# Optimization experiments

Measured on AMD Instinct MI355X. Metric: run time of the kernel, lower is better.

Reference implementation:

```python
import jax, jax.numpy as jnp
import numpy as np

# Mamba hyperparameters (match init_kwargs)
DIM = 384
D_STATE = 16
D_CONV = 4
EXPAND = 2
D_INNER = EXPAND * DIM            # 768
DT_RANK = (DIM + 15) // 16        # ceil(dim/16) = 24


def setup_inputs() -> dict:
    key = jax.random.key(0)
    ks = jax.random.split(key, 9)
    B = 4
    img_dims = (16, 16, 16)
    s = 0.02
    x = jax.random.normal(ks[0], (B, DIM) + img_dims, dtype=jnp.float32)
    # LayerNorm params
    gamma = jnp.ones((DIM,), jnp.float32)
    beta = jnp.zeros((DIM,), jnp.float32)
    # Mamba params (torch Linear layout: (out, in))
    W_in = jax.random.normal(ks[1], (2 * D_INNER, DIM), jnp.float32) * s
    conv_w = jax.random.normal(ks[2], (D_INNER, 1, D_CONV), jnp.float32) * (D_CONV ** -0.5)
    conv_b = jnp.zeros((D_INNER,), jnp.float32)
    W_xproj = jax.random.normal(ks[3], (DT_RANK + 2 * D_STATE, D_INNER), jnp.float32) * s
    W_dt = jax.random.normal(ks[4], (D_INNER, DT_RANK), jnp.float32) * (DT_RANK ** -0.5)
    # bias init so softplus(b_dt) gives small positive dt (~0.02), like mamba_ssm
    b_dt = jnp.full((D_INNER,), -4.0, jnp.float32) + jax.random.normal(ks[5], (D_INNER,), jnp.float32) * 0.1
    # S4D-real init: A = -[1..d_state] per channel
    A_log = jnp.log(jnp.broadcast_to(jnp.arange(1, D_STATE + 1, dtype=jnp.float32), (D_INNER, D_STATE)))
    D = jnp.ones((D_INNER,), jnp.float32)
    W_out = jax.random.normal(ks[6], (DIM, D_INNER), jnp.float32) * s
    return {"x": x, "gamma": gamma, "beta": beta, "W_in": W_in, "conv_w": conv_w,
            "conv_b": conv_b, "W_xproj": W_xproj, "W_dt": W_dt, "b_dt": b_dt,
            "A_log": A_log, "D": D, "W_out": W_out}


def _mamba_layer(x, gamma, beta, W_in, conv_w, conv_b, W_xproj, W_dt, b_dt, A_log, D, W_out):
    B, C = x.shape[0], x.shape[1]
    img_dims = x.shape[2:]
    L = int(np.prod(img_dims))
    xf = x.reshape(B, C, L).transpose(0, 2, 1)          # (B, L, C)

    # LayerNorm over channel dim
    mu = xf.mean(-1, keepdims=True)
    xc = xf - mu
    var = (xc * xc).mean(-1, keepdims=True)
    xn = xc * jax.lax.rsqrt(var + 1e-5) * gamma + beta   # (B, L, C)

    # in_proj -> x, z branches
    xz = xn @ W_in.T                                     # (B, L, 2*D_INNER)
    xm, z = jnp.split(xz, 2, axis=-1)

    # causal depthwise conv1d + SiLU
    xcv = xm.transpose(0, 2, 1)                          # (B, D_INNER, L)
    conv = jax.lax.conv_general_dilated(
        xcv, conv_w, window_strides=(1,), padding=[(D_CONV - 1, 0)],
        feature_group_count=D_INNER) + conv_b[None, :, None]
    xm = jax.nn.silu(conv.transpose(0, 2, 1))            # (B, L, D_INNER)

    # input-dependent dt, B, C
    dbl = xm @ W_xproj.T                                 # (B, L, DT_RANK + 2*D_STATE)
    dt, Bm, Cm = jnp.split(dbl, [DT_RANK, DT_RANK + D_STATE], axis=-1)
    delta = jax.nn.softplus(dt @ W_dt.T + b_dt)          # (B, L, D_INNER)
    A = -jnp.exp(A_log)                                  # (D_INNER, D_STATE)

    # selective scan over time (time-major)
    def step(h, inp):
        d_t, x_t, B_t, C_t = inp                         # (B,Din),(B,Din),(B,Dst),(B,Dst)
        dA = jnp.exp(d_t[..., None] * A)                 # (B, D_INNER, D_STATE)
        h = h * dA + (d_t * x_t)[..., None] * B_t[:, None, :]
        y = jnp.einsum('bds,bs->bd', h, C_t)
        return h, y

    h0 = jnp.zeros((B, D_INNER, D_STATE), xm.dtype)
    inps = (delta.transpose(1, 0, 2), xm.transpose(1, 0, 2),
            Bm.transpose(1, 0, 2), Cm.transpose(1, 0, 2))
    _, ys = jax.lax.scan(step, h0, inps)                 # (L, B, D_INNER)

    y = ys.transpose(1, 0, 2) + xm * D                   # skip via D
    y = y * jax.nn.silu(z)                               # gate
    out = y @ W_out.T                                    # (B, L, C)
    return out.transpose(0, 2, 1).reshape(x.shape)


def reference(x, gamma, beta, W_in, conv_w, conv_b, W_xproj, W_dt, b_dt, A_log, D, W_out):
    return _mamba_layer(x, gamma, beta, W_in, conv_w, conv_b, W_xproj, W_dt, b_dt, A_log, D, W_out)
```

## Files before the change

kernel.cpp:

```cpp
#include <hip/hip_runtime.h>

typedef short v8s __attribute__((ext_vector_type(8)));
typedef float v4f __attribute__((ext_vector_type(4)));

#define LSEQ   4096
#define BATCH  4
#define NDIM   384
#define DIN    768
#define DST    16
#define DTR    24
#define NTOK   (BATCH * LSEQ)
#define NCHUNK 128
#define CLEN   32
#define CT     8

__device__ __forceinline__ float b2f(unsigned short u) {
  unsigned int v = ((unsigned int)u) << 16;
  float f; __builtin_memcpy(&f, &v, 4); return f;
}
__device__ __forceinline__ unsigned short f2b(float f) {
  unsigned int x; __builtin_memcpy(&x, &f, 4);
  unsigned int r = x + 0x7FFFu + ((x >> 16) & 1u);
  return (unsigned short)(r >> 16);
}
__device__ __forceinline__ void gl2lds16(const void* g, void* l) {
  __builtin_amdgcn_global_load_lds(
      (const __attribute__((address_space(1))) void*)g,
      (__attribute__((address_space(3))) void*)l, 16, 0, 0);
}

__global__ __launch_bounds__(256) void cast_w(
    const float* __restrict__ a, unsigned short* __restrict__ oa, int na,
    const float* __restrict__ b, unsigned short* __restrict__ ob, int nb,
    const float* __restrict__ c, unsigned short* __restrict__ oc, int nc,
    const float* __restrict__ wdt, unsigned short* __restrict__ odt)
{
  int i = blockIdx.x * 256 + threadIdx.x;
  if (i < na) oa[i] = f2b(a[i]);
  if (i < nb) ob[i] = f2b(b[i]);
  if (i < nc) oc[i] = f2b(c[i]);
  if (i < DIN * 32) {
    int n = i >> 5, r = i & 31;
    odt[i] = (r < DTR) ? f2b(wdt[n * DTR + r]) : (unsigned short)0;
  }
}

__global__ __launch_bounds__(256) void ln_stats(
    const float* __restrict__ x, float* __restrict__ mu, float* __restrict__ rs)
{
  __shared__ float red[512];
  int blk = blockIdx.x;
  int b = blk >> 7, lc = blk & 127;
  int l0 = lc * 32;
  int t = threadIdx.x;
  int lt = t & 31, part = t >> 5;
  float s = 0.f, ss = 0.f;
  for (int c = part; c < NDIM; c += 8) {
    float v = x[((size_t)b * NDIM + c) * LSEQ + l0 + lt];
    s += v; ss += v * v;
  }
  red[part * 32 + lt] = s;
  red[256 + part * 32 + lt] = ss;
  __syncthreads();
  if (t < 32) {
    float sum = 0.f, ssum = 0.f;
    #pragma unroll
    for (int k = 0; k < 8; k++) { sum += red[k * 32 + t]; ssum += red[256 + k * 32 + t]; }
    float m = sum / (float)NDIM;
    float var = ssum / (float)NDIM - m * m;
    mu[(size_t)b * LSEQ + l0 + t] = m;
    rs[(size_t)b * LSEQ + l0 + t] = rsqrtf(var + 1e-5f);
  }
}

__global__ __launch_bounds__(256) void ln_apply(
    const float* __restrict__ x, const float* __restrict__ mu,
    const float* __restrict__ rs, const float* __restrict__ gamma,
    const float* __restrict__ beta, unsigned short* __restrict__ xn)
{
  __shared__ unsigned short tile[64 * 66];
  int blk = blockIdx.x;
  int ltb = blk & 63, ct = (blk >> 6) % 6, b = blk / (6 * 64);
  int l0 = ltb * 64, c0 = ct * 64;
  int t = threadIdx.x;
  int col = (t & 15) * 4;
  float4 mu4 = *(const float4*)(mu + (size_t)b * LSEQ + l0 + col);
  float4 rs4 = *(const float4*)(rs + (size_t)b * LSEQ + l0 + col);
  #pragma unroll
  for (int p = 0; p < 4; p++) {
    int row = (t >> 4) + p * 16;
    float g = gamma[c0 + row], be = beta[c0 + row];
    float4 v = *(const float4*)(x + ((size_t)b * NDIM + c0 + row) * LSEQ + l0 + col);
    unsigned int u0 = (unsigned int)f2b((v.x - mu4.x) * rs4.x * g + be)
                    | ((unsigned int)f2b((v.y - mu4.y) * rs4.y * g + be) << 16);
    unsigned int u1 = (unsigned int)f2b((v.z - mu4.z) * rs4.z * g + be)
                    | ((unsigned int)f2b((v.w - mu4.w) * rs4.w * g + be) << 16);
    *(unsigned int*)&tile[row * 66 + col]     = u0;
    *(unsigned int*)&tile[row * 66 + col + 2] = u1;
  }
  __syncthreads();
  for (int idx = t; idx < 64 * 64; idx += 256) {
    int l = idx >> 6, c = idx & 63;
    xn[((size_t)b * LSEQ + l0 + l) * NDIM + c0 + c] = tile[c * 66 + l];
  }
}

template <typename OT>
__global__ __launch_bounds__(256) void gemm128(
    const unsigned short* __restrict__ A, const unsigned short* __restrict__ W,
    OT* __restrict__ C, int K, int ldc)
{
  __shared__ short As[128 * 32];
  __shared__ short Ws[128 * 32];
  int t = threadIdx.x;
  int wave = t >> 6, lane = t & 63;
  int m0 = blockIdx.x * 128, n0 = blockIdx.y * 128;
  int wm = wave >> 1, wn = wave & 1;
  int lrow = lane & 15, quad = lane >> 4;
  int l4 = lane >> 2, p = lane & 3;
  int row0 = wave * 32 + l4;
  int row1 = row0 + 16;
  int k8 = p ^ (row0 & 3);
  int ldsoff0 = wave * 1024 + lane * 8;
  int ldsoff1 = ldsoff0 + 512;
  int swz = (lrow & 3) * 8;
  v4f acc[4][4];
  #pragma unroll
  for (int i = 0; i < 4; i++)
    #pragma unroll
    for (int j = 0; j < 4; j++) acc[i][j] = (v4f){0.f, 0.f, 0.f, 0.f};
  for (int kk = 0; kk < K; kk += 32) {
    gl2lds16(A + (size_t)(m0 + row0) * K + kk + k8 * 8, &As[ldsoff0]);
    gl2lds16(A + (size_t)(m0 + row1) * K + kk + k8 * 8, &As[ldsoff1]);
    gl2lds16(W + (size_t)(n0 + row0) * K + kk + k8 * 8, &Ws[ldsoff0]);
    gl2lds16(W + (size_t)(n0 + row1) * K + kk + k8 * 8, &Ws[ldsoff1]);
    __syncthreads();
    v8s af[4], bf[4];
    #pragma unroll
    for (int i = 0; i < 4; i++) {
      int ra = wm * 64 + i * 16 + lrow;
      af[i] = *(const v8s*)&As[ra * 32 + ((quad * 8) ^ swz)];
    }
    #pragma unroll
    for (int j = 0; j < 4; j++) {
      int rb = wn * 64 + j * 16 + lrow;
      bf[j] = *(const v8s*)&Ws[rb * 32 + ((quad * 8) ^ swz)];
    }
    #pragma unroll
    for (int i = 0; i < 4; i++)
      #pragma unroll
      for (int j = 0; j < 4; j++)
        acc[i][j] = __builtin_amdgcn_mfma_f32_16x16x32_bf16(af[i], bf[j], acc[i][j], 0, 0, 0);
    __syncthreads();
  }
  #pragma unroll
  for (int i = 0; i < 4; i++) {
    #pragma unroll
    for (int j = 0; j < 4; j++) {
      #pragma unroll
      for (int r = 0; r < 4; r++) {
        int m = m0 + wm * 64 + i * 16 + quad * 4 + r;
        int n = n0 + wn * 64 + j * 16 + lrow;
        if constexpr (sizeof(OT) == 4) C[(size_t)m * ldc + n] = acc[i][j][r];
        else                           C[(size_t)m * ldc + n] = (OT)f2b(acc[i][j][r]);
      }
    }
  }
}

#define LDK 40
__global__ __launch_bounds__(256) void gemm_bt64(
    const unsigned short* __restrict__ A, const unsigned short* __restrict__ W,
    unsigned short* __restrict__ C, int Nw, int K, int ldc)
{
  __shared__ short As[64 * LDK];
  __shared__ short Ws[64 * LDK];
  int m0 = blockIdx.x * 64, n0 = blockIdx.y * 64;
  int t = threadIdx.x;
  int wave = t >> 6, lane = t & 63;
  int lrow = lane & 15, quad = lane >> 4;
  int ldrow = t >> 2, ldcg = t & 3;
  v4f acc[4];
  #pragma unroll
  for (int j = 0; j < 4; j++) acc[j] = (v4f){0.f, 0.f, 0.f, 0.f};
  for (int kk = 0; kk < K; kk += 32) {
    v8s av = *(const v8s*)(A + (size_t)(m0 + ldrow) * K + kk + ldcg * 8);
    *(v8s*)&As[ldrow * LDK + ldcg * 8] = av;
    int wrow = n0 + ldrow;
    v8s wv = {0, 0, 0, 0, 0, 0, 0, 0};
    if (wrow < Nw) wv = *(const v8s*)(W + (size_t)wrow * K + kk + ldcg * 8);
    *(v8s*)&Ws[ldrow * LDK + ldcg * 8] = wv;
    __syncthreads();
    v8s afrag = *(const v8s*)&As[(wave * 16 + lrow) * LDK + quad * 8];
    #pragma unroll
    for (int j = 0; j < 4; j++) {
      v8s bfrag = *(const v8s*)&Ws[(j * 16 + lrow) * LDK + quad * 8];
      acc[j] = __builtin_amdgcn_mfma_f32_16x16x32_bf16(afrag, bfrag, acc[j], 0, 0, 0);
    }
    __syncthreads();
  }
  #pragma unroll
  for (int j = 0; j < 4; j++) {
    #pragma unroll
    for (int r = 0; r < 4; r++) {
      int m = m0 + wave * 16 + quad * 4 + r;
      int n = n0 + j * 16 + lrow;
      if (n < ldc) C[(size_t)m * ldc + n] = f2b(acc[j][r]);
    }
  }
}

__global__ __launch_bounds__(256) void dt_gemm(
    const unsigned short* __restrict__ A, const unsigned short* __restrict__ W,
    const float* __restrict__ b_dt, unsigned short* __restrict__ delta)
{
  __shared__ short As[128 * 32];
  __shared__ short Ws[128 * 32];
  int t = threadIdx.x;
  int wave = t >> 6, lane = t & 63;
  int m0 = blockIdx.x * 128, n0 = blockIdx.y * 128;
  int wm = wave >> 1, wn = wave & 1;
  int lrow = lane & 15, quad = lane >> 4;
  int l4 = lane >> 2, p = lane & 3;
  int row0 = wave * 32 + l4;
  int row1 = row0 + 16;
  int k8 = p ^ (row0 & 3);
  int ldsoff0 = wave * 1024 + lane * 8;
  int ldsoff1 = ldsoff0 + 512;
  int swz = (lrow & 3) * 8;
  gl2lds16(A + (size_t)(m0 + row0) * 64 + k8 * 8, &As[ldsoff0]);
  gl2lds16(A + (size_t)(m0 + row1) * 64 + k8 * 8, &As[ldsoff1]);
  gl2lds16(W + (size_t)(n0 + row0) * 32 + k8 * 8, &Ws[ldsoff0]);
  gl2lds16(W + (size_t)(n0 + row1) * 32 + k8 * 8, &Ws[ldsoff1]);
  __syncthreads();
  v4f acc[4][4];
  #pragma unroll
  for (int i = 0; i < 4; i++)
    #pragma unroll
    for (int j = 0; j < 4; j++) acc[i][j] = (v4f){0.f, 0.f, 0.f, 0.f};
  v8s af[4], bf[4];
  #pragma unroll
  for (int i = 0; i < 4; i++) {
    int ra = wm * 64 + i * 16 + lrow;
    af[i] = *(const v8s*)&As[ra * 32 + ((quad * 8) ^ swz)];
  }
  #pragma unroll
  for (int j = 0; j < 4; j++) {
    int rb = wn * 64 + j * 16 + lrow;
    bf[j] = *(const v8s*)&Ws[rb * 32 + ((quad * 8) ^ swz)];
  }
  #pragma unroll
  for (int i = 0; i < 4; i++)
    #pragma unroll
    for (int j = 0; j < 4; j++)
      acc[i][j] = __builtin_amdgcn_mfma_f32_16x16x32_bf16(af[i], bf[j], acc[i][j], 0, 0, 0);
  #pragma unroll
  for (int j = 0; j < 4; j++) {
    int n = n0 + wn * 64 + j * 16 + lrow;
    float bb = b_dt[n];
    #pragma unroll
    for (int i = 0; i < 4; i++) {
      #pragma unroll
      for (int r = 0; r < 4; r++) {
        int m = m0 + wm * 64 + i * 16 + quad * 4 + r;
        float a = acc[i][j][r] + bb;
        float sp = (a > 20.f) ? a : __logf(1.f + __expf(a));
        delta[(size_t)m * DIN + n] = f2b(sp);
      }
    }
  }
}

__global__ __launch_bounds__(256) void conv_silu_w(
    const unsigned short* __restrict__ xz, const float* __restrict__ conv_w,
    const float* __restrict__ conv_b, unsigned short* __restrict__ xc)
{
  int idx = blockIdx.x * 256 + threadIdx.x;
  int dg = idx % (DIN / 8);
  int bl0 = idx / (DIN / 8);
  int d = dg * 8;
  int t0 = bl0 * CT;
  int l0 = t0 & (LSEQ - 1);
  float w[4][8], bb[8];
  #pragma unroll
  for (int e = 0; e < 8; e++) {
    float4 we = *(const float4*)(conv_w + (size_t)(d + e) * 4);
    w[0][e] = we.x; w[1][e] = we.y; w[2][e] = we.z; w[3][e] = we.w;
  }
  {
    float4 b0 = *(const float4*)(conv_b + d);
    float4 b1 = *(const float4*)(conv_b + d + 4);
    bb[0] = b0.x; bb[1] = b0.y; bb[2] = b0.z; bb[3] = b0.w;
    bb[4] = b1.x; bb[5] = b1.y; bb[6] = b1.z; bb[7] = b1.w;
  }
  float xw[3][8];
  #pragma unroll
  for (int j = 0; j < 3; j++) {
    if (l0 - 3 + j >= 0) {
      v8s v = *(const v8s*)(xz + (size_t)(t0 - 3 + j) * (2 * DIN) + d);
      #pragma unroll
      for (int e = 0; e < 8; e++) xw[j][e] = b2f((unsigned short)v[e]);
    } else {
      #pragma unroll
      for (int e = 0; e < 8; e++) xw[j][e] = 0.f;
    }
  }
  for (int tt = 0; tt < CT; tt++) {
    v8s v = *(const v8s*)(xz + (size_t)(t0 + tt) * (2 * DIN) + d);
    float cur[8];
    #pragma unroll
    for (int e = 0; e < 8; e++) cur[e] = b2f((unsigned short)v[e]);
    v8s o;
    #pragma unroll
    for (int e = 0; e < 8; e++) {
      float acc = bb[e];
      acc = __builtin_fmaf(w[0][e], xw[0][e], acc);
      acc = __builtin_fmaf(w[1][e], xw[1][e], acc);
      acc = __builtin_fmaf(w[2][e], xw[2][e], acc);
      acc = __builtin_fmaf(w[3][e], cur[e], acc);
      float sig = 1.f / (1.f + __expf(-acc));
      o[e] = (short)f2b(acc * sig);
    }
    *(v8s*)(xc + (size_t)(t0 + tt) * DIN + d) = o;
    #pragma unroll
    for (int e = 0; e < 8; e++) {
      xw[0][e] = xw[1][e]; xw[1][e] = xw[2][e]; xw[2][e] = cur[e];
    }
  }
}

__global__ __launch_bounds__(256) void scan_a(
    const unsigned short* __restrict__ delta, const unsigned short* __restrict__ xc,
    const unsigned short* __restrict__ dbl, const float* __restrict__ A_log,
    float* __restrict__ P, float* __restrict__ H)
{
  __shared__ float BCf[CLEN * 32];
  int blk = blockIdx.x;
  int q = blk % 3, c = (blk / 3) % NCHUNK, b = blk / (3 * NCHUNK);
  int t = threadIdx.x;
  int d = q * 256 + t;
  if (t < CLEN * 4) {
    int tt = t >> 2, g = t & 3;
    v8s raw = *(const v8s*)(dbl + (size_t)(b * LSEQ + c * CLEN + tt) * 64 + DTR + g * 8);
    float* dst = &BCf[tt * 32 + g * 8];
    #pragma unroll
    for (int e = 0; e < 8; e++) dst[e] = b2f((unsigned short)raw[e]);
  }
  __syncthreads();
  float A_d[DST];
  bool fast = true;
  #pragma unroll
  for (int s = 0; s < DST; s++) {
    A_d[s] = -__expf(A_log[d * DST + s]);
    fast = fast && (__builtin_fabsf(A_d[s] + (float)(s + 1)) < 1e-3f * (s + 1));
  }
  float h[DST];
  #pragma unroll
  for (int s = 0; s < DST; s++) h[s] = 0.f;
  float S = 0.f;
  size_t base = ((size_t)b * LSEQ + c * CLEN) * DIN + d;
  if (fast) {
    for (int tt = 0; tt < CLEN; tt++) {
      float du = b2f(delta[base + (size_t)tt * DIN]);
      float xv = b2f(xc[base + (size_t)tt * DIN]);
      float dx = du * xv;
      S += du;
      float r = __expf(-du);
      float Bv[16];
      #pragma unroll
      for (int g = 0; g < 4; g++)
        *(float4*)&Bv[g * 4] = *(const float4*)&BCf[tt * 32 + g * 4];
      float a = r;
      #pragma unroll
      for (int s = 0; s < DST; s++) {
        h[s] = __builtin_fmaf(h[s], a, dx * Bv[s]);
        a *= r;
      }
    }
  } else {
    for (int tt = 0; tt < CLEN; tt++) {
      float du = b2f(delta[base + (size_t)tt * DIN]);
      float xv = b2f(xc[base + (size_t)tt * DIN]);
      float dx = du * xv;
      S += du;
      #pragma unroll
      for (int s = 0; s < DST; s++) {
        float a = __expf(du * A_d[s]);
        h[s] = h[s] * a + dx * BCf[tt * 32 + s];
      }
    }
  }
  size_t obase = (((size_t)b * NCHUNK + c) * DST) * DIN + d;
  if (fast) {
    float rS = __expf(-S), a = rS;
    #pragma unroll
    for (int s = 0; s < DST; s++) { P[obase + (size_t)s * DIN] = a; a *= rS; }
  } else {
    #pragma unroll
    for (int s = 0; s < DST; s++) P[obase + (size_t)s * DIN] = __expf(A_d[s] * S);
  }
  #pragma unroll
  for (int s = 0; s < DST; s++) H[obase + (size_t)s * DIN] = h[s];
}

__global__ __launch_bounds__(256) void scan_b(
    const float* __restrict__ P, const float* __restrict__ H, float* __restrict__ Hstart)
{
  int i = blockIdx.x * 256 + threadIdx.x;
  if (i >= BATCH * DST * DIN) return;
  int d = i % DIN;
  int s = (i / DIN) % DST;
  int b = i / (DST * DIN);
  float h = 0.f;
  for (int c = 0; c < NCHUNK; c++) {
    size_t idx = (((size_t)b * NCHUNK + c) * DST + s) * DIN + d;
    float p = P[idx];
    float hh = H[idx];
    Hstart[idx] = h;
    h = h * p + hh;
  }
}

__global__ __launch_bounds__(256) void scan_c(
    const unsigned short* __restrict__ delta, const unsigned short* __restrict__ xc,
    const unsigned short* __restrict__ dbl, const float* __restrict__ A_log,
    const float* __restrict__ Hstart, const unsigned short* __restrict__ xz,
    const float* __restrict__ Dp, unsigned short* __restrict__ ygate)
{
  __shared__ float BCf[CLEN * 32];
  int blk = blockIdx.x;
  int q = blk % 3, c = (blk / 3) % NCHUNK, b = blk / (3 * NCHUNK);
  int t = threadIdx.x;
  int d = q * 256 + t;
  if (t < CLEN * 4) {
    int tt = t >> 2, g = t & 3;
    v8s raw = *(const v8s*)(dbl + (size_t)(b * LSEQ + c * CLEN + tt) * 64 + DTR + g * 8);
    float* dst = &BCf[tt * 32 + g * 8];
    #pragma unroll
    for (int e = 0; e < 8; e++) dst[e] = b2f((unsigned short)raw[e]);
  }
  __syncthreads();
  float A_d[DST];
  bool fast = true;
  #pragma unroll
  for (int s = 0; s < DST; s++) {
    A_d[s] = -__expf(A_log[d * DST + s]);
    fast = fast && (__builtin_fabsf(A_d[s] + (float)(s + 1)) < 1e-3f * (s + 1));
  }
  size_t obase = (((size_t)b * NCHUNK + c) * DST) * DIN + d;
  float h[DST];
  #pragma unroll
  for (int s = 0; s < DST; s++) h[s] = Hstart[obase + (size_t)s * DIN];
  float Dv = Dp[d];
  size_t base = ((size_t)b * LSEQ + c * CLEN) * DIN + d;
  size_t zbase = ((size_t)b * LSEQ + c * CLEN) * (2 * DIN) + DIN + d;
  if (fast) {
    for (int tt = 0; tt < CLEN; tt++) {
      float du = b2f(delta[base + (size_t)tt * DIN]);
      float xv = b2f(xc[base + (size_t)tt * DIN]);
      float dx = du * xv;
      float r = __expf(-du);
      float Bv[16], Cv[16];
      #pragma unroll
      for (int g = 0; g < 4; g++) {
        *(float4*)&Bv[g * 4] = *(const float4*)&BCf[tt * 32 + g * 4];
        *(float4*)&Cv[g * 4] = *(const float4*)&BCf[tt * 32 + 16 + g * 4];
      }
      float a = r, y = 0.f;
      #pragma unroll
      for (int s = 0; s < DST; s++) {
        h[s] = __builtin_fmaf(h[s], a, dx * Bv[s]);
        y = __builtin_fmaf(h[s], Cv[s], y);
        a *= r;
      }
      float zv = b2f(xz[zbase + (size_t)tt * (2 * DIN)]);
      float g = zv / (1.f + __expf(-zv));
      float o = (y + xv * Dv) * g;
      ygate[base + (size_t)tt * DIN] = f2b(o);
    }
  } else {
    for (int tt = 0; tt < CLEN; tt++) {
      float du = b2f(delta[base + (size_t)tt * DIN]);
      float xv = b2f(xc[base + (size_t)tt * DIN]);
      float dx = du * xv;
      float y = 0.f;
      #pragma unroll
      for (int s = 0; s < DST; s++) {
        float a = __expf(du * A_d[s]);
        h[s] = h[s] * a + dx * BCf[tt * 32 + s];
        y += h[s] * BCf[tt * 32 + 16 + s];
      }
      float zv = b2f(xz[zbase + (size_t)tt * (2 * DIN)]);
      float g = zv / (1.f + __expf(-zv));
      float o = (y + xv * Dv) * g;
      ygate[base + (size_t)tt * DIN] = f2b(o);
    }
  }
}

__global__ __launch_bounds__(256) void transpose_out(
    const float* __restrict__ ytmp, float* __restrict__ out)
{
  __shared__ float tl[64][65];
  int blk = blockIdx.x;
  int ct = blk % 6, lt = (blk / 6) % 64, b = blk / (6 * 64);
  int t = threadIdx.x;
  int col = t & 63, row = t >> 6;
  for (int i = row; i < 64; i += 4)
    tl[i][col] = ytmp[((size_t)b * LSEQ + lt * 64 + i) * NDIM + ct * 64 + col];
  __syncthreads();
  for (int i = row; i < 64; i += 4)
    out[((size_t)b * NDIM + ct * 64 + i) * LSEQ + lt * 64 + col] = tl[col][i];
}

extern "C" void kernel_launch(void* const* d_in, const int* in_sizes, int n_in,
                              void* d_out, int out_size, void* d_ws, size_t ws_size,
                              hipStream_t stream) {
  const float* x      = (const float*)d_in[0];
  const float* gamma  = (const float*)d_in[1];
  const float* beta   = (const float*)d_in[2];
  const float* W_in   = (const float*)d_in[3];
  const float* conv_w = (const float*)d_in[4];
  const float* conv_b = (const float*)d_in[5];
  const float* W_xprj = (const float*)d_in[6];
  const float* W_dt   = (const float*)d_in[7];
  const float* b_dt   = (const float*)d_in[8];
  const float* A_log  = (const float*)d_in[9];
  const float* Dp     = (const float*)d_in[10];
  const float* W_out  = (const float*)d_in[11];
  float* out = (float*)d_out;

  char* ws = (char*)d_ws;
  size_t off = 0;
  auto take = [&](size_t bytes) -> char* {
    char* p = ws + off;
    off = (off + bytes + 255) & ~(size_t)255;
    return p;
  };
  const int NW_IN = 2 * DIN * NDIM;
  const int NW_XP = 56 * DIN;
  const int NW_OUT = NDIM * DIN;
  unsigned short* Wc_in  = (unsigned short*)take((size_t)NW_IN * 2);
  unsigned short* Wc_xp  = (unsigned short*)take((size_t)NW_XP * 2);
  unsigned short* Wc_out = (unsigned short*)take((size_t)NW_OUT * 2);
  unsigned short* Wc_dt  = (unsigned short*)take((size_t)DIN * 32 * 2);
  float*          mu    = (float*)take((size_t)NTOK * 4);
  float*          rsb   = (float*)take((size_t)NTOK * 4);
  unsigned short* xn    = (unsigned short*)take((size_t)NTOK * NDIM * 2);
  unsigned short* xz    = (unsigned short*)take((size_t)NTOK * 2 * DIN * 2);
  unsigned short* xc    = (unsigned short*)take((size_t)NTOK * DIN * 2);
  unsigned short* dbl   = (unsigned short*)take((size_t)NTOK * 64 * 2);
  unsigned short* delta = (unsigned short*)take((size_t)NTOK * DIN * 2);
  unsigned short* ygate = (unsigned short*)take((size_t)NTOK * DIN * 2);
  float*          P     = (float*)take((size_t)BATCH * NCHUNK * DST * DIN * 4);
  float*          H     = (float*)take((size_t)BATCH * NCHUNK * DST * DIN * 4);
  float*          Hst   = P;
  float*          ytmp  = (float*)delta;
  (void)ws_size; (void)in_sizes; (void)n_in; (void)out_size;

  cast_w<<<(NW_IN + 255) / 256, 256, 0, stream>>>(W_in, Wc_in, NW_IN,
                                                  W_xprj, Wc_xp, NW_XP,
                                                  W_out, Wc_out, NW_OUT,
                                                  W_dt, Wc_dt);
  ln_stats<<<BATCH * (LSEQ / 32), 256, 0, stream>>>(x, mu, rsb);
  ln_apply<<<BATCH * 6 * (LSEQ / 64), 256, 0, stream>>>(x, mu, rsb, gamma, beta, xn);
  gemm128<unsigned short><<<dim3(NTOK / 128, 1536 / 128), 256, 0, stream>>>(xn, Wc_in, xz, NDIM, 1536);
  conv_silu_w<<<(NTOK / CT) * (DIN / 8) / 256, 256, 0, stream>>>(xz, conv_w, conv_b, xc);
  gemm_bt64<<<dim3(NTOK / 64, 1), 256, 0, stream>>>(xc, Wc_xp, dbl, 56, DIN, 64);
  dt_gemm<<<dim3(NTOK / 128, DIN / 128), 256, 0, stream>>>(dbl, Wc_dt, b_dt, delta);
  scan_a<<<BATCH * NCHUNK * 3, 256, 0, stream>>>(delta, xc, dbl, A_log, P, H);
  scan_b<<<(BATCH * DST * DIN + 255) / 256, 256, 0, stream>>>(P, H, Hst);
  scan_c<<<BATCH * NCHUNK * 3, 256, 0, stream>>>(delta, xc, dbl, A_log, Hst, xz, Dp, ygate);
  gemm128<float><<<dim3(NTOK / 128, NDIM / 128), 256, 0, stream>>>(ygate, Wc_out, ytmp, DIN, NDIM);
  transpose_out<<<BATCH * 64 * 6, 256, 0, stream>>>(ytmp, out);
}
```

Measured before the change: 315.0 us.

## Fuse output transpose into out-proj GEMM and process two channels per scan thread

Adds a gemm_out kernel that computes W_out·ygateᵀ with swapped operands and writes straight into the channel-major output layout, which removes the fp32 ytmp buffer and the separate transpose kernel. The scan_a and scan_c kernels now use 128 threads, each handling two adjacent channels with packed 32-bit bf16 loads and stores, and all 128 threads cooperate on the B/C staging. This reduces kernel launches, global traffic and per-element load instructions. In exchange, the GEMM stores stride along L and may coalesce less well, and halving threads per block in the scan kernels raises register pressure and lowers parallelism.

```diff
diff --git a/kernel.cpp b/kernel.cpp
--- a/kernel.cpp
+++ b/kernel.cpp
@@ -17,6 +17,12 @@
 __device__ __forceinline__ float b2f(unsigned short u) {
   unsigned int v = ((unsigned int)u) << 16;
   float f; __builtin_memcpy(&f, &v, 4); return f;
+}
+__device__ __forceinline__ float blo(unsigned int w) {
+  unsigned int v = w << 16; float f; __builtin_memcpy(&f, &v, 4); return f;
+}
+__device__ __forceinline__ float bhi(unsigned int w) {
+  unsigned int v = w & 0xffff0000u; float f; __builtin_memcpy(&f, &v, 4); return f;
 }
 __device__ __forceinline__ unsigned short f2b(float f) {
   unsigned int x; __builtin_memcpy(&x, &f, 4);
@@ -163,6 +169,68 @@
         int n = n0 + wn * 64 + j * 16 + lrow;
         if constexpr (sizeof(OT) == 4) C[(size_t)m * ldc + n] = acc[i][j][r];
         else                           C[(size_t)m * ldc + n] = (OT)f2b(acc[i][j][r]);
+      }
+    }
+  }
+}
+
+__global__ __launch_bounds__(256) void gemm_out(
+    const unsigned short* __restrict__ A, const unsigned short* __restrict__ W,
+    float* __restrict__ out, int K)
+{
+  __shared__ short As[128 * 32];
+  __shared__ short Ws[128 * 32];
+  int t = threadIdx.x;
+  int wave = t >> 6, lane = t & 63;
+  int m0 = blockIdx.x * 128, n0 = blockIdx.y * 128;
+  int wm = wave >> 1, wn = wave & 1;
+  int lrow = lane & 15, quad = lane >> 4;
+  int l4 = lane >> 2, p = lane & 3;
+  int row0 = wave * 32 + l4;
+  int row1 = row0 + 16;
+  int k8 = p ^ (row0 & 3);
+  int ldsoff0 = wave * 1024 + lane * 8;
+  int ldsoff1 = ldsoff0 + 512;
+  int swz = (lrow & 3) * 8;
+  v4f acc[4][4];
+  #pragma unroll
+  for (int i = 0; i < 4; i++)
+    #pragma unroll
+    for (int j = 0; j < 4; j++) acc[i][j] = (v4f){0.f, 0.f, 0.f, 0.f};
+  for (int kk = 0; kk < K; kk += 32) {
+    gl2lds16(A + (size_t)(m0 + row0) * K + kk + k8 * 8, &As[ldsoff0]);
+    gl2lds16(A + (size_t)(m0 + row1) * K + kk + k8 * 8, &As[ldsoff1]);
+    gl2lds16(W + (size_t)(n0 + row0) * K + kk + k8 * 8, &Ws[ldsoff0]);
+    gl2lds16(W + (size_t)(n0 + row1) * K + kk + k8 * 8, &Ws[ldsoff1]);
+    __syncthreads();
+    v8s af[4], bf[4];
+    #pragma unroll
+    for (int i = 0; i < 4; i++) {
+      int ra = wm * 64 + i * 16 + lrow;
+      af[i] = *(const v8s*)&As[ra * 32 + ((quad * 8) ^ swz)];
+    }
+    #pragma unroll
+    for (int j = 0; j < 4; j++) {
+      int rb = wn * 64 + j * 16 + lrow;
+      bf[j] = *(const v8s*)&Ws[rb * 32 + ((quad * 8) ^ swz)];
+    }
+    #pragma unroll
+    for (int i = 0; i < 4; i++)
+      #pragma unroll
+      for (int j = 0; j < 4; j++)
+        acc[i][j] = __builtin_amdgcn_mfma_f32_16x16x32_bf16(af[i], bf[j], acc[i][j], 0, 0, 0);
+    __syncthreads();
+  }
+  #pragma unroll
+  for (int i = 0; i < 4; i++) {
+    #pragma unroll
+    for (int j = 0; j < 4; j++) {
+      #pragma unroll
+      for (int r = 0; r < 4; r++) {
+        int m = m0 + wm * 64 + i * 16 + quad * 4 + r;
+        int n = n0 + wn * 64 + j * 16 + lrow;
+        int b = n >> 12, l = n & (LSEQ - 1);
+        out[((size_t)b * NDIM + m) * LSEQ + l] = acc[i][j][r];
       }
     }
   }
@@ -329,7 +397,7 @@
   }
 }
 
-__global__ __launch_bounds__(256) void scan_a(
+__global__ __launch_bounds__(128) void scan_a(
     const unsigned short* __restrict__ delta, const unsigned short* __restrict__ xc,
     const unsigned short* __restrict__ dbl, const float* __restrict__ A_log,
     float* __restrict__ P, float* __restrict__ H)
@@ -338,8 +406,8 @@
   int blk = blockIdx.x;
   int q = blk % 3, c = (blk / 3) % NCHUNK, b = blk / (3 * NCHUNK);
   int t = threadIdx.x;
-  int d = q * 256 + t;
-  if (t < CLEN * 4) {
+  int d0 = q * 256 + 2 * t, d1 = d0 + 1;
+  {
     int tt = t >> 2, g = t & 3;
     v8s raw = *(const v8s*)(dbl + (size_t)(b * LSEQ + c * CLEN + tt) * 64 + DTR + g * 8);
     float* dst = &BCf[tt * 32 + g * 8];
@@ -347,60 +415,76 @@
     for (int e = 0; e < 8; e++) dst[e] = b2f((unsigned short)raw[e]);
   }
   __syncthreads();
-  float A_d[DST];
   bool fast = true;
   #pragma unroll
   for (int s = 0; s < DST; s++) {
-    A_d[s] = -__expf(A_log[d * DST + s]);
-    fast = fast && (__builtin_fabsf(A_d[s] + (float)(s + 1)) < 1e-3f * (s + 1));
-  }
-  float h[DST];
-  #pragma unroll
-  for (int s = 0; s < DST; s++) h[s] = 0.f;
-  float S = 0.f;
-  size_t base = ((size_t)b * LSEQ + c * CLEN) * DIN + d;
+    float a0 = __expf(A_log[d0 * DST + s]);
+    float a1 = __expf(A_log[d1 * DST + s]);
+    fast = fast && (__builtin_fabsf(a0 - (float)(s + 1)) < 1e-3f * (s + 1))
+                && (__builtin_fabsf(a1 - (float)(s + 1)) < 1e-3f * (s + 1));
+  }
+  float h0[DST], h1[DST];
+  #pragma unroll
+  for (int s = 0; s < DST; s++) { h0[s] = 0.f; h1[s] = 0.f; }
+  float S0 = 0.f, S1 = 0.f;
+  size_t base = ((size_t)b * LSEQ + c * CLEN) * DIN + d0;
+  size_t obase = (((size_t)b * NCHUNK + c) * DST) * DIN + d0;
   if (fast) {
     for (int tt = 0; tt < CLEN; tt++) {
-      float du = b2f(delta[base + (size_t)tt * DIN]);
-      float xv = b2f(xc[base + (size_t)tt * DIN]);
-      float dx = du * xv;
-      S += du;
-      float r = __expf(-du);
+      unsigned int wd = *(const unsigned int*)(delta + base + (size_t)tt * DIN);
+      unsigned int wx = *(const unsigned int*)(xc + base + (size_t)tt * DIN);
+      float du0 = blo(wd), du1 = bhi(wd);
+      float x0 = blo(wx), x1 = bhi(wx);
+      S0 += du0; S1 += du1;
+      float r0 = __expf(-du0), r1 = __expf(-du1);
+      float dx0 = du0 * x0, dx1 = du1 * x1;
       float Bv[16];
       #pragma unroll
       for (int g = 0; g < 4; g++)
         *(float4*)&Bv[g * 4] = *(const float4*)&BCf[tt * 32 + g * 4];
-      float a = r;
+      float a0 = r0, a1 = r1;
       #pragma unroll
       for (int s = 0; s < DST; s++) {
-        h[s] = __builtin_fmaf(h[s], a, dx * Bv[s]);
-        a *= r;
-      }
+        h0[s] = __builtin_fmaf(h0[s], a0, dx0 * Bv[s]);
+        h1[s] = __builtin_fmaf(h1[s], a1, dx1 * Bv[s]);
+        a0 *= r0; a1 *= r1;
+      }
+    }
+    float rS0 = __expf(-S0), rS1 = __expf(-S1);
+    float a0 = rS0, a1 = rS1;
+    #pragma unroll
+    for (int s = 0; s < DST; s++) {
+      *(float2*)&P[obase + (size_t)s * DIN] = (float2){a0, a1};
+      a0 *= rS0; a1 *= rS1;
     }
   } else {
+    float A0[DST], A1[DST];
+    #pragma unroll
+    for (int s = 0; s < DST; s++) {
+      A0[s] = -__expf(A_log[d0 * DST + s]);
+      A1[s] = -__expf(A_log[d1 * DST + s]);
+    }
     for (int tt = 0; tt < CLEN; tt++) {
-      float du = b2f(delta[base + (size_t)tt * DIN]);
-      float xv = b2f(xc[base + (size_t)tt * DIN]);
-      float dx = du * xv;
-      S += du;
+      unsigned int wd = *(const unsigned int*)(delta + base + (size_t)tt * DIN);
+      unsigned int wx = *(const unsigned int*)(xc + base + (size_t)tt * DIN);
+      float du0 = blo(wd), du1 = bhi(wd);
+      float x0 = blo(wx), x1 = bhi(wx);
+      S0 += du0; S1 += du1;
+      float dx0 = du0 * x0, dx1 = du1 * x1;
       #pragma unroll
       for (int s = 0; s < DST; s++) {
-        float a = __expf(du * A_d[s]);
-        h[s] = h[s] * a + dx * BCf[tt * 32 + s];
-      }
-    }
-  }
-  size_t obase = (((size_t)b * NCHUNK + c) * DST) * DIN + d;
-  if (fast) {
-    float rS = __expf(-S), a = rS;
-    #pragma unroll
-    for (int s = 0; s < DST; s++) { P[obase + (size_t)s * DIN] = a; a *= rS; }
-  } else {
-    #pragma unroll
-    for (int s = 0; s < DST; s++) P[obase + (size_t)s * DIN] = __expf(A_d[s] * S);
-  }
-  #pragma unroll
-  for (int s = 0; s < DST; s++) H[obase + (size_t)s * DIN] = h[s];
+        float Bs = BCf[tt * 32 + s];
+        h0[s] = h0[s] * __expf(du0 * A0[s]) + dx0 * Bs;
+        h1[s] = h1[s] * __expf(du1 * A1[s]) + dx1 * Bs;
+      }
+    }
+    #pragma unroll
+    for (int s = 0; s < DST; s++)
+      *(float2*)&P[obase + (size_t)s * DIN] = (float2){__expf(A0[s] * S0), __expf(A1[s] * S1)};
+  }
+  #pragma unroll
+  for (int s = 0; s < DST; s++)
+    *(float2*)&H[obase + (size_t)s * DIN] = (float2){h0[s], h1[s]};
 }
 
 __global__ __launch_bounds__(256) void scan_b(
@@ -421,7 +505,7 @@
   }
 }
 
-__global__ __launch_bounds__(256) void scan_c(
+__global__ __launch_bounds__(128) void scan_c(
     const unsigned short* __restrict__ delta, const unsigned short* __restrict__ xc,
     const unsigned short* __restrict__ dbl, const float* __restrict__ A_log,
     const float* __restrict__ Hstart, const unsigned short* __restrict__ xz,
@@ -431,8 +515,8 @@
   int blk = blockIdx.x;
   int q = blk % 3, c = (blk / 3) % NCHUNK, b = blk / (3 * NCHUNK);
   int t = threadIdx.x;
-  int d = q * 256 + t;
-  if (t < CLEN * 4) {
+  int d0 = q * 256 + 2 * t, d1 = d0 + 1;
+  {
     int tt = t >> 2, g = t & 3;
     v8s raw = *(const v8s*)(dbl + (size_t)(b * LSEQ + c * CLEN + tt) * 64 + DTR + g * 8);
     float* dst = &BCf[tt * 32 + g * 8];
@@ -440,77 +524,88 @@
     for (int e = 0; e < 8; e++) dst[e] = b2f((unsigned short)raw[e]);
   }
   __syncthreads();
-  float A_d[DST];
   bool fast = true;
   #pragma unroll
   for (int s = 0; s < DST; s++) {
-    A_d[s] = -__expf(A_log[d * DST + s]);
-    fast = fast && (__builtin_fabsf(A_d[s] + (float)(s + 1)) < 1e-3f * (s + 1));
-  }
-  size_t obase = (((size_t)b * NCHUNK + c) * DST) * DIN + d;
-  float h[DST];
-  #pragma unroll
-  for (int s = 0; s < DST; s++) h[s] = Hstart[obase + (size_t)s * DIN];
-  float Dv = Dp[d];
-  size_t base = ((size_t)b * LSEQ + c * CLEN) * DIN + d;
-  size_t zbase = ((size_t)b * LSEQ + c * CLEN) * (2 * DIN) + DIN + d;
+    float a0 = __expf(A_log[d0 * DST + s]);
+    float a1 = __expf(A_log[d1 * DST + s]);
+    fast = fast && (__builtin_fabsf(a0 - (float)(s + 1)) < 1e-3f * (s + 1))
+                && (__builtin_fabsf(a1 - (float)(s + 1)) < 1e-3f * (s + 1));
+  }
+  size_t obase = (((size_t)b * NCHUNK + c) * DST) * DIN + d0;
+  float h0[DST], h1[DST];
+  #pragma unroll
+  for (int s = 0; s < DST; s++) {
+    float2 hs = *(const float2*)&Hstart[obase + (size_t)s * DIN];
+    h0[s] = hs.x; h1[s] = hs.y;
+  }
+  float Dv0 = Dp[d0], Dv1 = Dp[d1];
+  size_t base = ((size_t)b * LSEQ + c * CLEN) * DIN + d0;
+  size_t zbase = ((size_t)b * LSEQ + c * CLEN) * (2 * DIN) + DIN + d0;
   if (fast) {
     for (int tt = 0; tt < CLEN; tt++) {
-      float du = b2f(delta[base + (size_t)tt * DIN]);
-      float xv = b2f(xc[base + (size_t)tt * DIN]);
-      float dx = du * xv;
-      float r = __expf(-du);
+      unsigned int wd = *(const unsigned int*)(delta + base + (size_t)tt * DIN);
+      unsigned int wx = *(const unsigned int*)(xc + base + (size_t)tt * DIN);
+      float du0 = blo(wd), du1 = bhi(wd);
+      float x0 = blo(wx), x1 = bhi(wx);
+      float dx0 = du0 * x0, dx1 = du1 * x1;
+      float r0 = __expf(-du0), r1 = __expf(-du1);
       float Bv[16], Cv[16];
       #pragma unroll
       for (int g = 0; g < 4; g++) {
         *(float4*)&Bv[g * 4] = *(const float4*)&BCf[tt * 32 + g * 4];
         *(float4*)&Cv[g * 4] = *(const float4*)&BCf[tt * 32 + 16 + g * 4];
       }
-      float a = r, y = 0.f;
+      float a0 = r0, a1 = r1, y0 = 0.f, y1 = 0.f;
       #pragma unroll
       for (int s = 0; s < DST; s++) {
-        h[s] = __builtin_fmaf(h[s], a, dx * Bv[s]);
-        y = __builtin_fmaf(h[s], Cv[s], y);
-        a *= r;
-      }
-      float zv = b2f(xz[zbase + (size_t)tt * (2 * DIN)]);
-      float g = zv / (1.f + __expf(-zv));
-      float o = (y + xv * Dv) * g;
-      ygate[base + (size_t)tt * DIN] = f2b(o);
+        h0[s] = __builtin_fmaf(h0[s], a0, dx0 * Bv[s]);
+        h1[s] = __builtin_fmaf(h1[s], a1, dx1 * Bv[s]);
+        y0 = __builtin_fmaf(h0[s], Cv[s], y0);
+        y1 = __builtin_fmaf(h1[s], Cv[s], y1);
+        a0 *= r0; a1 *= r1;
+      }
+      unsigned int wz = *(const unsigned int*)(xz + zbase + (size_t)tt * (2 * DIN));
+      float z0 = blo(wz), z1 = bhi(wz);
+      float g0 = z0 / (1.f + __expf(-z0));
+      float g1 = z1 / (1.f + __expf(-z1));
+      float o0 = (y0 + x0 * Dv0) * g0;
+      float o1 = (y1 + x1 * Dv1) * g1;
+      unsigned int ow = (unsigned int)f2b(o0) | ((unsigned int)f2b(o1) << 16);
+      *(unsigned int*)(ygate + base + (size_t)tt * DIN) = ow;
     }
   } else {
+    float A0[DST], A1[DST];
+    #pragma unroll
+    for (int s = 0; s < DST; s++) {
+      A0[s] = -__expf(A_log[d0 * DST + s]);
+      A1[s] = -__expf(A_log[d1 * DST + s]);
+    }
     for (int tt = 0; tt < CLEN; tt++) {
-      float du = b2f(delta[base + (size_t)tt * DIN]);
-      float xv = b2f(xc[base + (size_t)tt * DIN]);
-      float dx = du * xv;
-      float y = 0.f;
+      unsigned int wd = *(const unsigned int*)(delta + base + (size_t)tt * DIN);
+      unsigned int wx = *(const unsigned int*)(xc + base + (size_t)tt * DIN);
+      float du0 = blo(wd), du1 = bhi(wd);
+      float x0 = blo(wx), x1 = bhi(wx);
+      float dx0 = du0 * x0, dx1 = du1 * x1;
+      float y0 = 0.f, y1 = 0.f;
       #pragma unroll
       for (int s = 0; s < DST; s++) {
-        float a = __expf(du * A_d[s]);
-        h[s] = h[s] * a + dx * BCf[tt * 32 + s];
-        y += h[s] * BCf[tt * 32 + 16 + s];
-      }
-      float zv = b2f(xz[zbase + (size_t)tt * (2 * DIN)]);
-      float g = zv / (1.f + __expf(-zv));
-      float o = (y + xv * Dv) * g;
-      ygate[base + (size_t)tt * DIN] = f2b(o);
-    }
-  }
-}
-
-__global__ __launch_bounds__(256) void transpose_out(
-    const float* __restrict__ ytmp, float* __restrict__ out)
-{
-  __shared__ float tl[64][65];
-  int blk = blockIdx.x;
-  int ct = blk % 6, lt = (blk / 6) % 64, b = blk / (6 * 64);
-  int t = threadIdx.x;
-  int col = t & 63, row = t >> 6;
-  for (int i = row; i < 64; i += 4)
-    tl[i][col] = ytmp[((size_t)b * LSEQ + lt * 64 + i) * NDIM + ct * 64 + col];
-  __syncthreads();
-  for (int i = row; i < 64; i += 4)
-    out[((size_t)b * NDIM + ct * 64 + i) * LSEQ + lt * 64 + col] = tl[col][i];
+        float Bs = BCf[tt * 32 + s], Cs = BCf[tt * 32 + 16 + s];
+        h0[s] = h0[s] * __expf(du0 * A0[s]) + dx0 * Bs;
+        h1[s] = h1[s] * __expf(du1 * A1[s]) + dx1 * Bs;
+        y0 += h0[s] * Cs;
+        y1 += h1[s] * Cs;
+      }
+      unsigned int wz = *(const unsigned int*)(xz + zbase + (size_t)tt * (2 * DIN));
+      float z0 = blo(wz), z1 = bhi(wz);
+      float g0 = z0 / (1.f + __expf(-z0));
+      float g1 = z1 / (1.f + __expf(-z1));
+      float o0 = (y0 + x0 * Dv0) * g0;
+      float o1 = (y1 + x1 * Dv1) * g1;
+      unsigned int ow = (unsigned int)f2b(o0) | ((unsigned int)f2b(o1) << 16);
+      *(unsigned int*)(ygate + base + (size_t)tt * DIN) = ow;
+    }
+  }
 }
 
 extern "C" void kernel_launch(void* const* d_in, const int* in_sizes, int n_in,
@@ -555,7 +650,6 @@
   float*          P     = (float*)take((size_t)BATCH * NCHUNK * DST * DIN * 4);
   float*          H     = (float*)take((size_t)BATCH * NCHUNK * DST * DIN * 4);
   float*          Hst   = P;
-  float*          ytmp  = (float*)delta;
   (void)ws_size; (void)in_sizes; (void)n_in; (void)out_size;
 
   cast_w<<<(NW_IN + 255) / 256, 256, 0, stream>>>(W_in, Wc_in, NW_IN,
@@ -568,9 +662,8 @@
   conv_silu_w<<<(NTOK / CT) * (DIN / 8) / 256, 256, 0, stream>>>(xz, conv_w, conv_b, xc);
   gemm_bt64<<<dim3(NTOK / 64, 1), 256, 0, stream>>>(xc, Wc_xp, dbl, 56, DIN, 64);
   dt_gemm<<<dim3(NTOK / 128, DIN / 128), 256, 0, stream>>>(dbl, Wc_dt, b_dt, delta);
-  scan_a<<<BATCH * NCHUNK * 3, 256, 0, stream>>>(delta, xc, dbl, A_log, P, H);
+  scan_a<<<BATCH * NCHUNK * 3, 128, 0, stream>>>(delta, xc, dbl, A_log, P, H);
   scan_b<<<(BATCH * DST * DIN + 255) / 256, 256, 0, stream>>>(P, H, Hst);
-  scan_c<<<BATCH * NCHUNK * 3, 256, 0, stream>>>(delta, xc, dbl, A_log, Hst, xz, Dp, ygate);
-  gemm128<float><<<dim3(NTOK / 128, NDIM / 128), 256, 0, stream>>>(ygate, Wc_out, ytmp, DIN, NDIM);
-  transpose_out<<<BATCH * 64 * 6, 256, 0, stream>>>(ytmp, out);
-}
+  scan_c<<<BATCH * NCHUNK * 3, 128, 0, stream>>>(delta, xc, dbl, A_log, Hst, xz, Dp, ygate);
+  gemm_out<<<dim3(NDIM / 128, NTOK / 128), 256, 0, stream>>>(Wc_out, ygate, out, DIN);
+}
```

New measurement: 360.1 us. 1.14x slower.
